# Kernel optimization log

Hardware: AMD Instinct MI355X
Metric: run time of the kernel (lower is better)

Reference implementation:

```python
import jax, jax.numpy as jnp
import numpy as np

NUM_CLASSES = 100000   # vocab (input_dim of the layer)
DIM = 256              # embedding dim (output_dim of the layer)
BATCH = 256
NUM_TRUE = 1024        # hardcoded num_true in call()
NUM_SAMPLED = 16384    # hardcoded num_sampled in call()
LOG_RANGE = float(np.log(NUM_CLASSES + 1.0))


def _sample_log_uniform_unique(rng, n, range_max):
    # Mimics tf log_uniform_candidate_sampler with unique=True: rejection-sample
    # from P(c) ~ log((c+2)/(c+1)) until n unique ids are collected.
    seen = {}
    log_range = np.log(range_max + 1.0)
    while len(seen) < n:
        u = rng.uniform(0.0, log_range, size=2 * n)
        ids = np.minimum(np.floor(np.exp(u) - 1.0).astype(np.int64), range_max - 1)
        for v in ids.tolist():
            if len(seen) >= n:
                break
            seen[v] = None
    return np.fromiter(seen.keys(), dtype=np.int64, count=n)


def setup_inputs() -> dict:
    key = jax.random.key(0)
    k1, k2, k3, k4 = jax.random.split(key, 4)
    inputs = jax.random.normal(k1, (BATCH, DIM), jnp.float32)
    # Original inits w/b to zeros; use small random values for a non-degenerate baseline.
    w = jax.random.normal(k2, (NUM_CLASSES, DIM), jnp.float32) * 0.02
    b = jax.random.normal(k3, (NUM_CLASSES,), jnp.float32) * 0.02
    labels = jax.random.randint(k4, (BATCH, NUM_TRUE), 0, NUM_CLASSES, dtype=jnp.int32)
    rng = np.random.default_rng(0)
    sampled = jnp.asarray(_sample_log_uniform_unique(rng, NUM_SAMPLED, NUM_CLASSES), jnp.int32)
    return {"inputs": inputs, "w": w, "b": b, "labels": labels, "sampled": sampled}


def _log_uniform_prob(ids):
    idf = ids.astype(jnp.float32)
    return jnp.log((idf + 2.0) / (idf + 1.0)) / LOG_RANGE


def _expected_count(ids):
    # P(id appears among NUM_SAMPLED unique candidates) = 1 - (1-p)^NUM_SAMPLED
    p = _log_uniform_prob(ids)
    return -jnp.expm1(NUM_SAMPLED * jnp.log1p(-p))


def _sigmoid_xent(logits, target):
    # numerically stable sigmoid cross-entropy, target is a scalar label value
    return jnp.maximum(logits, 0.0) - logits * target + jnp.log1p(jnp.exp(-jnp.abs(logits)))


def reference(inputs, w, b, labels, sampled):
    # true logits: per-example dot with each true class row  [B, T]
    true_w = w[labels]                                    # [B, T, D] gather
    true_logits = jnp.einsum('bd,btd->bt', inputs, true_w) + b[labels]
    true_logits = true_logits - jnp.log(_expected_count(labels))
    # sampled logits: shared candidate set  [B, S]
    sampled_logits = inputs @ w[sampled].T + b[sampled]
    sampled_logits = sampled_logits - jnp.log(_expected_count(sampled))
    # NCE targets: 1/num_true for true classes, 0 for sampled; sum over columns
    true_xent = _sigmoid_xent(true_logits, 1.0 / NUM_TRUE)
    sampled_xent = _sigmoid_xent(sampled_logits, 0.0)
    return true_xent.sum(axis=1) + sampled_xent.sum(axis=1)   # [B]
```

## Files before the change

kernel.cpp:

```cpp
#include <hip/hip_runtime.h>
#include <hip/hip_bf16.h>

#define NUM_CLASSES 100000
#define DIM 256
#define BATCH 256
#define NUM_TRUE 1024
#define NUM_SAMPLED 16384
#define LOG_RANGE 11.51293546492023f
#define INV_LOG_RANGE (1.0f / LOG_RANGE)

#define SWEEP_BLOCKS 1563
#define CLS_PAD 100032

typedef __bf16 bf16x8 __attribute__((ext_vector_type(8)));
typedef float  f32x4  __attribute__((ext_vector_type(4)));

static __device__ __forceinline__ unsigned short f2bf(float f) {
    unsigned int u = __float_as_uint(f);
    unsigned int lsb = (u >> 16) & 1u;
    u += 0x7fffu + lsb;
    return (unsigned short)(u >> 16);
}

static __device__ __forceinline__ float neg_log_ec_fast(int id) {
    float idf = (float)id;
    float e = 1.0f / (idf + 1.0f);
    float p = log1pf(e) * INV_LOG_RANGE;
    float q = p * (1.0f + 0.5f * p + 0.3333333f * p * p);
    float ec = 1.0f - __expf(-(float)NUM_SAMPLED * q);
    return -__logf(ec);
}

__global__ __launch_bounds__(256) void scatter_kernel(const int* __restrict__ labels,
                                                      const int* __restrict__ sampled,
                                                      const float* __restrict__ inputs,
                                                      unsigned int* __restrict__ table,
                                                      unsigned char* __restrict__ flags,
                                                      unsigned short* __restrict__ inbf) {
    const int gid = blockIdx.x * 256 + threadIdx.x;
    const int c = labels[gid];
    const int b = gid >> 10;
    atomicAdd(&table[c * 32 + (b >> 3)], 1u << ((b & 7) * 4));
    if (gid < NUM_SAMPLED) {
        flags[sampled[gid]] = 1;
        float4 v = ((const float4*)inputs)[gid];
        ushort4 p;
        p.x = f2bf(v.x); p.y = f2bf(v.y); p.z = f2bf(v.z); p.w = f2bf(v.w);
        ((ushort4*)inbf)[gid] = p;
    }
}

__global__ __launch_bounds__(256) void sweep_kernel(const float* __restrict__ w,
                                                    const float* __restrict__ bias,
                                                    const unsigned int* __restrict__ table,
                                                    const unsigned char* __restrict__ flags,
                                                    const unsigned short* __restrict__ inbf,
                                                    float* __restrict__ partial) {
    __shared__ unsigned short lw[32][264];
    __shared__ unsigned int lmask[32][32];
    __shared__ float cs[32];
    __shared__ float sf[32];
    __shared__ float bacc[BATCH];

    const int tid  = threadIdx.x;
    const int lane = tid & 63;
    const int wv   = tid >> 6;
    const int m    = lane & 15;
    const int quad = lane >> 4;

    const unsigned short* bbase = inbf + (wv * 64 + m) * DIM + quad * 8;
    bf16x8 bfc[8], bfn[8];
    #pragma unroll
    for (int kk = 0; kk < 8; ++kk) bfc[kk] = *(const bf16x8*)(bbase + kk * 32);

    #pragma unroll 1
    for (int p = 0; p < 2; ++p) {
        const int c0 = blockIdx.x * 64 + p * 32;

        #pragma unroll
        for (int k = 0; k < 8; ++k) {
            const int lrow = (tid >> 6) + k * 4;
            const int col  = (tid & 63) * 4;
            int frow = c0 + lrow;
            frow = frow < NUM_CLASSES ? frow : NUM_CLASSES - 1;
            float4 v = *(const float4*)(w + (size_t)frow * DIM + col);
            ushort4 pk;
            pk.x = f2bf(v.x); pk.y = f2bf(v.y); pk.z = f2bf(v.z); pk.w = f2bf(v.w);
            *(ushort4*)(&lw[lrow][col]) = pk;
        }
        ((int4*)&lmask[0][0])[tid] = ((const int4*)(table + (size_t)c0 * 32))[tid];
        if (tid < 32) {
            const int c = c0 + tid;
            const int cc = c < NUM_CLASSES ? c : NUM_CLASSES - 1;
            cs[tid] = bias[cc] + neg_log_ec_fast(c);
            sf[tid] = flags[c] ? 1.0f : 0.0f;
        }
        __syncthreads();

        bf16x8 af[2][8];
        #pragma unroll
        for (int s = 0; s < 2; ++s)
            #pragma unroll
            for (int kk = 0; kk < 8; ++kk)
                af[s][kk] = *(const bf16x8*)(&lw[s * 16 + m][kk * 32 + quad * 8]);

        #pragma unroll
        for (int tt = 0; tt < 4; ++tt) {
            {
                const unsigned short* bp = bbase + (((tt + 1) & 3) * 16) * DIM;
                #pragma unroll
                for (int kk = 0; kk < 8; ++kk) bfn[kk] = *(const bf16x8*)(bp + kk * 32);
            }
            f32x4 a0 = {0, 0, 0, 0}, a1 = {0, 0, 0, 0};
            #pragma unroll
            for (int kk = 0; kk < 8; ++kk) {
                a0 = __builtin_amdgcn_mfma_f32_16x16x32_bf16(af[0][kk], bfc[kk], a0, 0, 0, 0);
                a1 = __builtin_amdgcn_mfma_f32_16x16x32_bf16(af[1][kk], bfc[kk], a1, 0, 0, 0);
            }
            const int widx = wv * 8 + tt * 2 + (m >> 3);
            const int nsh  = (m & 7) * 4;
            float ps = 0.0f;
            #pragma unroll
            for (int r = 0; r < 4; ++r) {
                {
                    const int cl = quad * 4 + r;
                    float l = a0[r] + cs[cl];
                    float kf = (float)((lmask[cl][widx] >> nsh) & 15u);
                    float base = fmaxf(l, 0.0f) + __logf(1.0f + __expf(-fabsf(l)));
                    ps += (kf + sf[cl]) * base - kf * l * (1.0f / (float)NUM_TRUE);
                }
                {
                    const int cl = 16 + quad * 4 + r;
                    float l = a1[r] + cs[cl];
                    float kf = (float)((lmask[cl][widx] >> nsh) & 15u);
                    float base = fmaxf(l, 0.0f) + __logf(1.0f + __expf(-fabsf(l)));
                    ps += (kf + sf[cl]) * base - kf * l * (1.0f / (float)NUM_TRUE);
                }
            }
            ps += __shfl_xor(ps, 16); ps += __shfl_xor(ps, 32);
            if (quad == 0) {
                const int bi = wv * 64 + tt * 16 + m;
                if (p == 0) bacc[bi] = ps; else bacc[bi] += ps;
            }
            #pragma unroll
            for (int kk = 0; kk < 8; ++kk) bfc[kk] = bfn[kk];
        }
        __syncthreads();
    }
    partial[(size_t)blockIdx.x * BATCH + tid] = bacc[tid];
}

__global__ __launch_bounds__(256) void reduce_kernel(const float* __restrict__ partial,
                                                     float* __restrict__ out) {
    __shared__ float wsum[4];
    const int b = blockIdx.x;
    const int tid = threadIdx.x;
    float v = 0.0f;
    for (int j = tid; j < SWEEP_BLOCKS; j += 256)
        v += partial[(size_t)j * BATCH + b];
    v += __shfl_xor(v, 1);  v += __shfl_xor(v, 2);  v += __shfl_xor(v, 4);
    v += __shfl_xor(v, 8);  v += __shfl_xor(v, 16); v += __shfl_xor(v, 32);
    if ((tid & 63) == 0) wsum[tid >> 6] = v;
    __syncthreads();
    if (tid == 0) out[b] = wsum[0] + wsum[1] + wsum[2] + wsum[3];
}

extern "C" void kernel_launch(void* const* d_in, const int* in_sizes, int n_in,
                              void* d_out, int out_size, void* d_ws, size_t ws_size,
                              hipStream_t stream) {
    const float* inputs  = (const float*)d_in[0];
    const float* w       = (const float*)d_in[1];
    const float* bias    = (const float*)d_in[2];
    const int*   labels  = (const int*)d_in[3];
    const int*   sampled = (const int*)d_in[4];
    float* out = (float*)d_out;

    unsigned int*   table   = (unsigned int*)d_ws;
    unsigned char*  flags   = (unsigned char*)d_ws + 12804096;
    unsigned short* inbf    = (unsigned short*)((char*)d_ws + 12904128);
    float*          partial = (float*)((char*)d_ws + 13035200);

    hipMemsetAsync(d_ws, 0, 12904128, stream);
    scatter_kernel<<<(BATCH * NUM_TRUE) / 256, 256, 0, stream>>>(labels, sampled, inputs,
                                                                 table, flags, inbf);
    sweep_kernel<<<SWEEP_BLOCKS, 256, 0, stream>>>(w, bias, table, flags, inbf, partial);
    reduce_kernel<<<BATCH, 256, 0, stream>>>(partial, out);
}
```

Before: 209.4 us.

## Restructure sweep into single-wave blocks loading W directly into registers

The sweep kernel now runs 64-thread single-wave blocks, each owning 32 classes and looping over all 256 batch rows. It drops the LDS staging of W by loading fp32 rows straight into MFMA operand registers with bf16 conversion, and pads the mask table in shared memory to avoid bank conflicts. This doubles the block count and the partial buffer that the reduce kernel must sum. It also gives up the register prefetch of the next input tile and the sharing of W tiles across four waves.

```diff
diff --git a/kernel.cpp b/kernel.cpp
--- a/kernel.cpp
+++ b/kernel.cpp
@@ -9,8 +9,7 @@
 #define LOG_RANGE 11.51293546492023f
 #define INV_LOG_RANGE (1.0f / LOG_RANGE)
 
-#define SWEEP_BLOCKS 1563
-#define CLS_PAD 100032
+#define SWEEP_BLOCKS 3126
 
 typedef __bf16 bf16x8 __attribute__((ext_vector_type(8)));
 typedef float  f32x4  __attribute__((ext_vector_type(4)));
@@ -50,104 +49,94 @@
     }
 }
 
-__global__ __launch_bounds__(256) void sweep_kernel(const float* __restrict__ w,
-                                                    const float* __restrict__ bias,
-                                                    const unsigned int* __restrict__ table,
-                                                    const unsigned char* __restrict__ flags,
-                                                    const unsigned short* __restrict__ inbf,
-                                                    float* __restrict__ partial) {
-    __shared__ unsigned short lw[32][264];
-    __shared__ unsigned int lmask[32][32];
+__global__ __launch_bounds__(64, 3) void sweep_kernel(const float* __restrict__ w,
+                                                      const float* __restrict__ bias,
+                                                      const unsigned int* __restrict__ table,
+                                                      const unsigned char* __restrict__ flags,
+                                                      const unsigned short* __restrict__ inbf,
+                                                      float* __restrict__ partial) {
+    __shared__ unsigned int lmask[32][33];
     __shared__ float cs[32];
     __shared__ float sf[32];
     __shared__ float bacc[BATCH];
 
-    const int tid  = threadIdx.x;
-    const int lane = tid & 63;
-    const int wv   = tid >> 6;
+    const int lane = threadIdx.x;
     const int m    = lane & 15;
     const int quad = lane >> 4;
+    const int c0   = blockIdx.x * 32;
 
-    const unsigned short* bbase = inbf + (wv * 64 + m) * DIM + quad * 8;
-    bf16x8 bfc[8], bfn[8];
+    {
+        const unsigned int* src = table + (size_t)c0 * 32;
+        #pragma unroll
+        for (int i = 0; i < 16; ++i) {
+            const int idx = i * 64 + lane;
+            lmask[idx >> 5][idx & 31] = src[idx];
+        }
+    }
+    if (lane < 32) {
+        const int c = c0 + lane;
+        const int cc = c < NUM_CLASSES ? c : NUM_CLASSES - 1;
+        cs[lane] = bias[cc] + neg_log_ec_fast(c);
+        sf[lane] = flags[c] ? 1.0f : 0.0f;
+    }
+
+    bf16x8 af[2][8];
     #pragma unroll
-    for (int kk = 0; kk < 8; ++kk) bfc[kk] = *(const bf16x8*)(bbase + kk * 32);
+    for (int s = 0; s < 2; ++s) {
+        int row = c0 + s * 16 + m;
+        row = row < NUM_CLASSES ? row : NUM_CLASSES - 1;
+        const float* wr = w + (size_t)row * DIM + quad * 8;
+        #pragma unroll
+        for (int kk = 0; kk < 8; ++kk) {
+            float4 v0 = *(const float4*)(wr + kk * 32);
+            float4 v1 = *(const float4*)(wr + kk * 32 + 4);
+            union { unsigned short u[8]; bf16x8 b; } t;
+            t.u[0] = f2bf(v0.x); t.u[1] = f2bf(v0.y); t.u[2] = f2bf(v0.z); t.u[3] = f2bf(v0.w);
+            t.u[4] = f2bf(v1.x); t.u[5] = f2bf(v1.y); t.u[6] = f2bf(v1.z); t.u[7] = f2bf(v1.w);
+            af[s][kk] = t.b;
+        }
+    }
+    __syncthreads();
 
     #pragma unroll 1
-    for (int p = 0; p < 2; ++p) {
-        const int c0 = blockIdx.x * 64 + p * 32;
-
+    for (int tt = 0; tt < 16; ++tt) {
+        const unsigned short* bp = inbf + (tt * 16 + m) * DIM + quad * 8;
+        bf16x8 bf[8];
         #pragma unroll
-        for (int k = 0; k < 8; ++k) {
-            const int lrow = (tid >> 6) + k * 4;
-            const int col  = (tid & 63) * 4;
-            int frow = c0 + lrow;
-            frow = frow < NUM_CLASSES ? frow : NUM_CLASSES - 1;
-            float4 v = *(const float4*)(w + (size_t)frow * DIM + col);
-            ushort4 pk;
-            pk.x = f2bf(v.x); pk.y = f2bf(v.y); pk.z = f2bf(v.z); pk.w = f2bf(v.w);
-            *(ushort4*)(&lw[lrow][col]) = pk;
+        for (int kk = 0; kk < 8; ++kk) bf[kk] = *(const bf16x8*)(bp + kk * 32);
+        f32x4 a0 = {0, 0, 0, 0}, a1 = {0, 0, 0, 0};
+        #pragma unroll
+        for (int kk = 0; kk < 8; ++kk) {
+            a0 = __builtin_amdgcn_mfma_f32_16x16x32_bf16(af[0][kk], bf[kk], a0, 0, 0, 0);
+            a1 = __builtin_amdgcn_mfma_f32_16x16x32_bf16(af[1][kk], bf[kk], a1, 0, 0, 0);
         }
-        ((int4*)&lmask[0][0])[tid] = ((const int4*)(table + (size_t)c0 * 32))[tid];
-        if (tid < 32) {
-            const int c = c0 + tid;
-            const int cc = c < NUM_CLASSES ? c : NUM_CLASSES - 1;
-            cs[tid] = bias[cc] + neg_log_ec_fast(c);
-            sf[tid] = flags[c] ? 1.0f : 0.0f;
+        const int widx = tt * 2 + (m >> 3);
+        const int nsh  = (m & 7) * 4;
+        float ps = 0.0f;
+        #pragma unroll
+        for (int r = 0; r < 4; ++r) {
+            {
+                const int cl = quad * 4 + r;
+                float l = a0[r] + cs[cl];
+                float kf = (float)((lmask[cl][widx] >> nsh) & 15u);
+                float base = fmaxf(l, 0.0f) + __logf(1.0f + __expf(-fabsf(l)));
+                ps += (kf + sf[cl]) * base - kf * l * (1.0f / (float)NUM_TRUE);
+            }
+            {
+                const int cl = 16 + quad * 4 + r;
+                float l = a1[r] + cs[cl];
+                float kf = (float)((lmask[cl][widx] >> nsh) & 15u);
+                float base = fmaxf(l, 0.0f) + __logf(1.0f + __expf(-fabsf(l)));
+                ps += (kf + sf[cl]) * base - kf * l * (1.0f / (float)NUM_TRUE);
+            }
         }
-        __syncthreads();
-
-        bf16x8 af[2][8];
-        #pragma unroll
-        for (int s = 0; s < 2; ++s)
-            #pragma unroll
-            for (int kk = 0; kk < 8; ++kk)
-                af[s][kk] = *(const bf16x8*)(&lw[s * 16 + m][kk * 32 + quad * 8]);
-
-        #pragma unroll
-        for (int tt = 0; tt < 4; ++tt) {
-            {
-                const unsigned short* bp = bbase + (((tt + 1) & 3) * 16) * DIM;
-                #pragma unroll
-                for (int kk = 0; kk < 8; ++kk) bfn[kk] = *(const bf16x8*)(bp + kk * 32);
-            }
-            f32x4 a0 = {0, 0, 0, 0}, a1 = {0, 0, 0, 0};
-            #pragma unroll
-            for (int kk = 0; kk < 8; ++kk) {
-                a0 = __builtin_amdgcn_mfma_f32_16x16x32_bf16(af[0][kk], bfc[kk], a0, 0, 0, 0);
-                a1 = __builtin_amdgcn_mfma_f32_16x16x32_bf16(af[1][kk], bfc[kk], a1, 0, 0, 0);
-            }
-            const int widx = wv * 8 + tt * 2 + (m >> 3);
-            const int nsh  = (m & 7) * 4;
-            float ps = 0.0f;
-            #pragma unroll
-            for (int r = 0; r < 4; ++r) {
-                {
-                    const int cl = quad * 4 + r;
-                    float l = a0[r] + cs[cl];
-                    float kf = (float)((lmask[cl][widx] >> nsh) & 15u);
-                    float base = fmaxf(l, 0.0f) + __logf(1.0f + __expf(-fabsf(l)));
-                    ps += (kf + sf[cl]) * base - kf * l * (1.0f / (float)NUM_TRUE);
-                }
-                {
-                    const int cl = 16 + quad * 4 + r;
-                    float l = a1[r] + cs[cl];
-                    float kf = (float)((lmask[cl][widx] >> nsh) & 15u);
-                    float base = fmaxf(l, 0.0f) + __logf(1.0f + __expf(-fabsf(l)));
-                    ps += (kf + sf[cl]) * base - kf * l * (1.0f / (float)NUM_TRUE);
-                }
-            }
-            ps += __shfl_xor(ps, 16); ps += __shfl_xor(ps, 32);
-            if (quad == 0) {
-                const int bi = wv * 64 + tt * 16 + m;
-                if (p == 0) bacc[bi] = ps; else bacc[bi] += ps;
-            }
-            #pragma unroll
-            for (int kk = 0; kk < 8; ++kk) bfc[kk] = bfn[kk];
-        }
-        __syncthreads();
+        ps += __shfl_xor(ps, 16); ps += __shfl_xor(ps, 32);
+        if (quad == 0) bacc[tt * 16 + m] = ps;
     }
-    partial[(size_t)blockIdx.x * BATCH + tid] = bacc[tid];
+    __syncthreads();
+    #pragma unroll
+    for (int i = 0; i < 4; ++i)
+        partial[(size_t)blockIdx.x * BATCH + i * 64 + lane] = bacc[i * 64 + lane];
 }
 
 __global__ __launch_bounds__(256) void reduce_kernel(const float* __restrict__ partial,
@@ -183,6 +172,6 @@
     hipMemsetAsync(d_ws, 0, 12904128, stream);
     scatter_kernel<<<(BATCH * NUM_TRUE) / 256, 256, 0, stream>>>(labels, sampled, inputs,
                                                                  table, flags, inbf);
-    sweep_kernel<<<SWEEP_BLOCKS, 256, 0, stream>>>(w, bias, table, flags, inbf, partial);
+    sweep_kernel<<<SWEEP_BLOCKS, 64, 0, stream>>>(w, bias, table, flags, inbf, partial);
     reduce_kernel<<<BATCH, 256, 0, stream>>>(partial, out);
 }
```

New measurement: 239.2 us. 1.14x slower.
